# Optimization experiments

Hardware: AMD Instinct MI355X
Metric: run time of the kernel (lower is better)

The kernel has to match this reference:

```python
import jax, jax.numpy as jnp
import numpy as np

B, S, IN_DIM, OUT_DIM = 4, 2048, 1024, 1024
NEG = -9e15

def _xavier(key, shape, gain=1.414):
    fan_in, fan_out = shape[0], shape[1]
    a = gain * np.sqrt(6.0 / (fan_in + fan_out))
    return jax.random.uniform(key, shape, jnp.float32, -a, a)

def setup_inputs() -> dict:
    key = jax.random.key(0)
    ks = jax.random.split(key, 8)
    x = jax.random.normal(ks[0], (B, S, IN_DIM), jnp.float32)
    W_query = _xavier(ks[1], (IN_DIM, OUT_DIM))
    W_key = _xavier(ks[2], (IN_DIM, OUT_DIM))
    W_value = _xavier(ks[3], (IN_DIM, OUT_DIM))
    # torch Linear default init (kaiming-uniform-ish); values don't matter for correctness baseline
    W1 = _xavier(ks[4], (OUT_DIM + IN_DIM, OUT_DIM), gain=1.0)
    b1 = jnp.zeros((OUT_DIM,), jnp.float32)
    W2 = _xavier(ks[5], (OUT_DIM, OUT_DIM), gain=1.0)
    b2 = jnp.zeros((OUT_DIM,), jnp.float32)
    return {"x": x, "W_query": W_query, "W_key": W_key, "W_value": W_value,
            "W1": W1, "b1": b1, "W2": W2, "b2": b2}

def reference(x, W_query, W_key, W_value, W1, b1, W2, b2):
    # QKV projections: [B,S,in] @ [in,out] -> [B,S,out]
    q = jnp.einsum('bsi,io->bso', x, W_query)
    k = jnp.einsum('bsi,io->bso', x, W_key)
    v = jnp.einsum('bsi,io->bso', x, W_value)
    scale = 1.0 / jnp.sqrt(jnp.float32(OUT_DIM))
    e = jnp.einsum('bqd,bkd->bqk', q, k) * scale  # [B,S,S]
    causal = jnp.tril(jnp.ones((S, S), jnp.float32))  # mask > 0 keeps lower triangle
    attn = jnp.where(causal > 0, e, jnp.float32(NEG))
    attn = jax.nn.softmax(attn, axis=2)
    # dropout: eval mode (train=False) -> identity
    out = jnp.einsum('bqk,bkd->bqd', attn, v)  # [B,S,out]
    h = jnp.concatenate([out, x], axis=-1)  # [B,S,out+in]
    h = jax.nn.relu(jnp.einsum('bsf,fo->bso', h, W1) + b1)
    return jnp.einsum('bsf,fo->bso', h, W2) + b2
```

## Files before the change

### kernel.cpp

```cpp
#include <hip/hip_runtime.h>
#include <stdint.h>

typedef __attribute__((ext_vector_type(8))) short short8;
typedef __attribute__((ext_vector_type(4))) short short4v;
typedef __attribute__((ext_vector_type(4))) float f32x4;

__device__ __forceinline__ unsigned short f32_to_bf16(float f) {
    unsigned int u = __float_as_uint(f);
    u += 0x7FFFu + ((u >> 16) & 1u);
    return (unsigned short)(u >> 16);
}

__device__ __forceinline__ short8 load8_f32_as_bf16(const float* __restrict__ ap) {
    f32x4 f0 = *(const f32x4*)ap;
    f32x4 f1 = *(const f32x4*)(ap + 4);
    union { short8 s; unsigned short u[8]; } cv;
#pragma unroll
    for (int t = 0; t < 4; ++t) {
        cv.u[t]     = f32_to_bf16(f0[t]);
        cv.u[t + 4] = f32_to_bf16(f1[t]);
    }
    return cv.s;
}

__device__ __forceinline__ void gld_lds16(const void* g, void* l) {
    __builtin_amdgcn_global_load_lds(
        (const __attribute__((address_space(1))) unsigned int*)(unsigned long long)(uintptr_t)g,
        (__attribute__((address_space(3))) unsigned int*)(unsigned int)(uintptr_t)l,
        16, 0, 0);
}

template<int AMODE, int EPI, int SWIZ, bool KLIMIT, int MT>
__global__ __launch_bounds__(256, 4)
void gemm128(const unsigned short* __restrict__ A, const unsigned short* __restrict__ A2,
             int lda, int lda2, int ksplit,
             const unsigned short* __restrict__ B, int ldb,
             void* __restrict__ C, int ldc, int K,
             long aStride, long bStride, long cStride,
             const float* __restrict__ bias, long biasStride, float scale,
             void* __restrict__ C2, int ldc2)
{
    int z = blockIdx.z;
    int mblk, nblk;
    if (SWIZ == 6) {
        int x = blockIdx.x, yy = blockIdx.y;
        if (z < 2) { mblk = x * 8 + (yy & 7); nblk = yy >> 3; }
        else       { nblk = x * 8 + (yy & 7); mblk = yy >> 3; }
    } else {
        mblk = blockIdx.y;
        nblk = blockIdx.x;
    }
    int m0 = mblk * MT;
    int n0 = nblk * 128;

    const unsigned short* Ab;
    const unsigned short* Bb;
    if (SWIZ == 6) {
        if (z < 2) { Ab = A; Bb = B + (size_t)z * bStride; }
        else       { Ab = B + (size_t)2 * bStride; Bb = A; }
    } else {
        Ab = A + (size_t)z * aStride;
        Bb = B + (size_t)z * bStride;
    }

    __shared__ __align__(16) short As[MT * 64];
    __shared__ __align__(16) short Bs[128 * 64];

    int tid  = threadIdx.x;
    int lane = tid & 63, wid = tid >> 6;
    constexpr int MI = MT / 32;
    int wm = (wid & 1) * (MT / 2), wn = (wid >> 1) * 64;
    int fr = lane & 15, fq = lane >> 4;
    int sw0 = ((fq    ) ^ (fr & 7)) * 16;
    int sw1 = ((fq ^ 4) ^ (fr & 7)) * 16;

    int rS = tid >> 3;
    int cS = ((tid & 7) ^ (rS & 7)) * 8;
    char* AsB = (char*)As; char* BsB = (char*)Bs;

    int kend = KLIMIT ? min(K, m0 + MT) : K;

    f32x4 acc[MI][4];
#pragma unroll
    for (int i = 0; i < MI; ++i)
#pragma unroll
    for (int j = 0; j < 4; ++j) acc[i][j] = f32x4{0.f, 0.f, 0.f, 0.f};

    for (int k0 = 0; k0 < kend; k0 += 64) {
        const unsigned short* Asrc = Ab;
        int koff = k0, ldax = lda;
        if (AMODE == 2 && k0 >= ksplit) { Asrc = A2; koff = k0 - ksplit; ldax = lda2; }
        const unsigned short* pa = Asrc + (size_t)(m0 + rS) * ldax + koff + cS;
        const unsigned short* pb = Bb   + (size_t)(n0 + rS) * ldb  + k0   + cS;
#pragma unroll
        for (int t = 0; t < MT / 32; ++t)
            gld_lds16(pa + (size_t)(32 * t) * ldax, AsB + t * 4096 + tid * 16);
#pragma unroll
        for (int t = 0; t < 4; ++t)
            gld_lds16(pb + (size_t)(32 * t) * ldb,  BsB + t * 4096 + tid * 16);
        __syncthreads();

#pragma unroll
        for (int kh = 0; kh < 2; ++kh) {
            int sw = kh ? sw1 : sw0;
            short8 a[MI], b[4];
#pragma unroll
            for (int i = 0; i < MI; ++i)
                a[i] = *(const short8*)(AsB + (wm + i * 16 + fr) * 128 + sw);
#pragma unroll
            for (int j = 0; j < 4; ++j)
                b[j] = *(const short8*)(BsB + (wn + j * 16 + fr) * 128 + sw);
#pragma unroll
            for (int i = 0; i < MI; ++i)
#pragma unroll
            for (int j = 0; j < 4; ++j)
                acc[i][j] = __builtin_amdgcn_mfma_f32_16x16x32_bf16(a[i], b[j], acc[i][j], 0, 0, 0);
        }
        __syncthreads();
    }

    if (EPI == 0) {
        unsigned short* Cz; int ldcz;
        if (SWIZ == 6 && z >= 2) { Cz = (unsigned short*)C2; ldcz = ldc2; }
        else { Cz = (unsigned short*)C + (size_t)z * cStride; ldcz = ldc; }
#pragma unroll
        for (int i = 0; i < MI; ++i)
#pragma unroll
        for (int j = 0; j < 4; ++j)
#pragma unroll
        for (int r = 0; r < 4; ++r) {
            int row = m0 + wm + i * 16 + fq * 4 + r;
            int col = n0 + wn + j * 16 + fr;
            Cz[(size_t)row * ldcz + col] = f32_to_bf16(acc[i][j][r]);
        }
    }
}

template<int AMODE, int EPI, int SWIZ, bool KLIMIT>
__global__ __launch_bounds__(256, 2)
void gemmdb(const unsigned short* __restrict__ A, const unsigned short* __restrict__ A2,
            int lda, int lda2, int ksplit,
            const unsigned short* __restrict__ B, int ldb,
            void* __restrict__ C, int ldc, int K,
            long aStride, long bStride, long cStride,
            const float* __restrict__ bias, long biasStride, float scale)
{
    int z = blockIdx.z;
    int mblk, nblk;
    if (SWIZ == 1) {
        int lin = blockIdx.y * gridDim.x + blockIdx.x;
        int mchunk = gridDim.y >> 3;
        int xcd = lin & 7, idx = lin >> 3;
        mblk = xcd * mchunk + idx % mchunk;
        nblk = idx / mchunk;
    } else if (SWIZ == 5) {
        int x = blockIdx.x;
        int per = (int)gridDim.x >> 3;
        x = (x & 7) * per + (x >> 3);
        int a = (int)sqrtf(2.f * (float)x + 1.f);
        if (a > 15) a = 15;
        while (a < 15 && ((a + 1) * (a + 2) / 2) <= x) ++a;
        while (a > 0 && (a * (a + 1) / 2) > x) --a;
        mblk = a;
        nblk = x - a * (a + 1) / 2;
    } else if (SWIZ == 7) {
        int glin = (int)blockIdx.z * 128 + (int)blockIdx.y * 8 + (int)blockIdx.x;
        int xcd = glin & 7;
        int s   = glin >> 3;
        z = xcd >> 1;
        int h  = xcd & 1;
        int jm = s & 7;
        nblk   = s >> 3;
        mblk   = (jm & 1) ? (15 - h - (jm >> 1) * 2) : ((jm >> 1) * 2 + h);
    } else {
        mblk = blockIdx.y;
        nblk = blockIdx.x;
    }
    int m0 = mblk * 128;
    int n0 = nblk * 128;

    const unsigned short* Ab = A + (size_t)z * aStride;
    const unsigned short* Bb = B + (size_t)z * bStride;

    __shared__ __align__(16) char lds[65536];

    int tid  = threadIdx.x;
    int lane = tid & 63, wid = tid >> 6;
    int wm = (wid & 1) * 64, wn = (wid >> 1) * 64;
    int fr = lane & 15, fq = lane >> 4;
    int sw0 = ((fq    ) ^ (fr & 7)) * 16;
    int sw1 = ((fq ^ 4) ^ (fr & 7)) * 16;

    int rS = tid >> 3;
    int cS = ((tid & 7) ^ (rS & 7)) * 8;

    int kend = KLIMIT ? min(K, m0 + 128) : K;
    int NT = kend >> 6;

    f32x4 acc[4][4];
#pragma unroll
    for (int i = 0; i < 4; ++i)
#pragma unroll
    for (int j = 0; j < 4; ++j) acc[i][j] = f32x4{0.f, 0.f, 0.f, 0.f};

    auto STAGE = [&](int kt) {
        char* dst = lds + (kt & 1) * 32768;
        const unsigned short* Asrc = Ab; int koff = kt << 6; int ldax = lda;
        if (AMODE == 2 && koff >= ksplit) { Asrc = A2; koff -= ksplit; ldax = lda2; }
        const unsigned short* pa = Asrc + (size_t)(m0 + rS) * ldax + koff + cS;
        const unsigned short* pb = Bb   + (size_t)(n0 + rS) * ldb + (kt << 6) + cS;
#pragma unroll
        for (int u = 0; u < 4; ++u)
            gld_lds16(pa + (size_t)(32 * u) * ldax, dst + u * 4096 + tid * 16);
#pragma unroll
        for (int u = 0; u < 4; ++u)
            gld_lds16(pb + (size_t)(32 * u) * ldb, dst + 16384 + u * 4096 + tid * 16);
    };

    STAGE(0);
    for (int t = 0; t < NT; ++t) {
        if (t + 1 < NT) {
            STAGE(t + 1);
            asm volatile("s_waitcnt vmcnt(8)" ::: "memory");
        } else {
            asm volatile("s_waitcnt vmcnt(0)" ::: "memory");
        }
        __builtin_amdgcn_s_barrier();
        __builtin_amdgcn_sched_barrier(0);
        const char* AsB = (const char*)lds + (t & 1) * 32768;
        const char* BsB = AsB + 16384;
#pragma unroll
        for (int kh = 0; kh < 2; ++kh) {
            int sw = kh ? sw1 : sw0;
            short8 a[4], b[4];
#pragma unroll
            for (int i = 0; i < 4; ++i)
                a[i] = *(const short8*)(AsB + (wm + i * 16 + fr) * 128 + sw);
#pragma unroll
            for (int j = 0; j < 4; ++j)
                b[j] = *(const short8*)(BsB + (wn + j * 16 + fr) * 128 + sw);
            __builtin_amdgcn_s_setprio(1);
#pragma unroll
            for (int i = 0; i < 4; ++i)
#pragma unroll
            for (int j = 0; j < 4; ++j)
                acc[i][j] = __builtin_amdgcn_mfma_f32_16x16x32_bf16(a[i], b[j], acc[i][j], 0, 0, 0);
            __builtin_amdgcn_s_setprio(0);
        }
        __builtin_amdgcn_s_barrier();
        __builtin_amdgcn_sched_barrier(0);
        asm volatile("" ::: "memory");
    }

    if (EPI == 6) {
        unsigned short* Cz = (unsigned short*)C + (size_t)z * cStride;
        float* rs = const_cast<float*>(bias) + z * biasStride;
#pragma unroll
        for (int i = 0; i < 4; ++i)
#pragma unroll
        for (int r = 0; r < 4; ++r) {
            int row = m0 + wm + i * 16 + fq * 4 + r;
            float s = 0.f;
#pragma unroll
            for (int j = 0; j < 4; ++j) {
                int col = n0 + wn + j * 16 + fr;
                float e = (col <= row) ? __expf(acc[i][j][r] * scale - 16.f) : 0.f;
                s += e;
                Cz[(size_t)row * ldc + col] = f32_to_bf16(e);
            }
            s += __shfl_xor(s, 1);
            s += __shfl_xor(s, 2);
            s += __shfl_xor(s, 4);
            s += __shfl_xor(s, 8);
            if (fr == 0) atomicAdd(&rs[row], s);
        }
    } else if (EPI == 4) {
        unsigned short* Cz = (unsigned short*)C + (size_t)z * cStride;
#pragma unroll
        for (int i = 0; i < 4; ++i)
#pragma unroll
        for (int r = 0; r < 4; ++r) {
            int row = m0 + wm + i * 16 + fq * 4 + r;
            float inv = 1.f / bias[z * biasStride + row];
#pragma unroll
            for (int j = 0; j < 4; ++j) {
                int col = n0 + wn + j * 16 + fr;
                Cz[(size_t)row * ldc + col] = f32_to_bf16(acc[i][j][r] * inv);
            }
        }
    } else {
#pragma unroll
        for (int i = 0; i < 4; ++i)
#pragma unroll
        for (int j = 0; j < 4; ++j)
#pragma unroll
        for (int r = 0; r < 4; ++r) {
            int row = m0 + wm + i * 16 + fq * 4 + r;
            int col = n0 + wn + j * 16 + fr;
            float v = acc[i][j][r];
            if (EPI == 2) {
                v += bias[col];
                v = v > 0.f ? v : 0.f;
                ((unsigned short*)C + (size_t)z * cStride)[(size_t)row * ldc + col] = f32_to_bf16(v);
            } else {
                ((float*)C + (size_t)z * cStride)[(size_t)row * ldc + col] = v + bias[col];
            }
        }
    }
}

__device__ __forceinline__ void transpose_tile64(const float* __restrict__ in,
                                                 unsigned short* __restrict__ out,
                                                 int rows, int cols, int bx, int by, int tid)
{
    __shared__ float t[64][65];
    int tx = tid & 15, ty = tid >> 4;
    int r0 = by * 64, c0 = bx * 64;
#pragma unroll
    for (int i = 0; i < 4; ++i) {
        f32x4 v = *(const f32x4*)(in + (size_t)(r0 + ty + i * 16) * cols + c0 + tx * 4);
#pragma unroll
        for (int j = 0; j < 4; ++j) t[ty + i * 16][tx * 4 + j] = v[j];
    }
    __syncthreads();
#pragma unroll
    for (int i = 0; i < 4; ++i) {
        union { short4v s; unsigned short u[4]; } o;
#pragma unroll
        for (int j = 0; j < 4; ++j) o.u[j] = f32_to_bf16(t[tx * 4 + j][ty + i * 16]);
        *(short4v*)(out + (size_t)(c0 + ty + i * 16) * rows + r0 + tx * 4) = o.s;
    }
}

__global__ __launch_bounds__(256)
void prep_kernel(const float* __restrict__ x,
                 const float* __restrict__ Wq, const float* __restrict__ Wk,
                 const float* __restrict__ Wv, const float* __restrict__ W1,
                 const float* __restrict__ W2,
                 unsigned short* __restrict__ xb, unsigned short* __restrict__ WT,
                 unsigned short* __restrict__ W1T, unsigned short* __restrict__ W2T,
                 float* __restrict__ rsum)
{
    int idx = blockIdx.x;
    int tid = threadIdx.x;
    if (idx < 1024) {
#pragma unroll
        for (int it = 0; it < 4; ++it) {
            size_t i = ((size_t)idx * 4 + it) * 2048 + (size_t)tid * 8;
            *(short8*)(xb + i) = load8_f32_as_bf16(x + i);
        }
    } else if (idx < 1792) {
        int t = idx - 1024;
        int w = t >> 8; t &= 255;
        const float* in = w == 0 ? Wq : (w == 1 ? Wk : Wv);
        transpose_tile64(in, WT + (size_t)w * 1024 * 1024, 1024, 1024,
                         t & 15, t >> 4, tid);
    } else if (idx < 2304) {
        int t = idx - 1792;
        transpose_tile64(W1, W1T, 2048, 1024, t & 15, t >> 4, tid);
    } else if (idx < 2560) {
        int t = idx - 2304;
        transpose_tile64(W2, W2T, 1024, 1024, t & 15, t >> 4, tid);
    } else {
        int t = idx - 2560;
        f32x4 zero = {0.f, 0.f, 0.f, 0.f};
        float* p = rsum + ((size_t)t * 256 + tid) * 8;
        *(f32x4*)p = zero;
        *(f32x4*)(p + 4) = zero;
    }
}

extern "C" void kernel_launch(void* const* d_in, const int* in_sizes, int n_in,
                              void* d_out, int out_size, void* d_ws, size_t ws_size,
                              hipStream_t stream)
{
    const float* x  = (const float*)d_in[0];
    const float* Wq = (const float*)d_in[1];
    const float* Wk = (const float*)d_in[2];
    const float* Wv = (const float*)d_in[3];
    const float* W1 = (const float*)d_in[4];
    const float* b1 = (const float*)d_in[5];
    const float* W2 = (const float*)d_in[6];
    const float* b2 = (const float*)d_in[7];
    float* out = (float*)d_out;

    size_t off = 0;
    auto alloc = [&](size_t bytes) {
        char* r = (char*)d_ws + off;
        off += (bytes + 255) & ~(size_t)255;
        return r;
    };
    const size_t TOK = (size_t)8192 * 1024;
    unsigned short* WT   = (unsigned short*)alloc((size_t)3072 * 1024 * 2);
    unsigned short* W1T  = (unsigned short*)alloc((size_t)1024 * 2048 * 2);
    unsigned short* W2T  = (unsigned short*)alloc((size_t)1024 * 1024 * 2);
    unsigned short* xb   = (unsigned short*)alloc(TOK * 2);
    unsigned short* vT   = (unsigned short*)alloc((size_t)1024 * 8192 * 2);
    unsigned short* attn = (unsigned short*)alloc(TOK * 2);
    float*          rsum = (float*)         alloc((size_t)4 * 2048 * 4);
    unsigned short* q    = (unsigned short*)alloc(TOK * 2);
    unsigned short* k    = (unsigned short*)alloc(TOK * 2);
    unsigned short* S    = (unsigned short*)alloc((size_t)4 * 2048 * 2048 * 2);
    unsigned short* h1   = S;

    prep_kernel<<<2564, 256, 0, stream>>>(x, Wq, Wk, Wv, W1, W2, xb, WT, W1T, W2T, rsum);

    gemm128<0, 0, 6, false, 128><<<dim3(8, 64, 3), 256, 0, stream>>>(
        xb, nullptr, 1024, 0, 0, WT, 1024, q, 1024, 1024,
        0, (long)1024 * 1024, (long)TOK, nullptr, 0, 0.f, vT, 8192);

    gemmdb<0, 6, 5, false><<<dim3(136, 1, 4), 256, 0, stream>>>(
        q, nullptr, 1024, 0, 0, k, 1024, S, 2048, 1024,
        (long)2048 * 1024, (long)2048 * 1024, (long)2048 * 2048, rsum, 2048, 0.03125f);

    gemmdb<0, 4, 7, true><<<dim3(8, 16, 4), 256, 0, stream>>>(
        S, nullptr, 2048, 0, 0, vT, 8192, attn, 1024, 2048,
        (long)2048 * 2048, (long)2048, (long)2048 * 1024, rsum, 2048, 0.f);

    gemmdb<2, 2, 1, false><<<dim3(8, 64, 1), 256, 0, stream>>>(
        attn, xb, 1024, 1024, 1024, W1T, 2048, h1, 1024, 2048,
        0, 0, 0, b1, 0, 0.f);

    gemmdb<0, 3, 1, false><<<dim3(8, 64, 1), 256, 0, stream>>>(
        h1, nullptr, 1024, 0, 0, W2T, 1024, out, 1024, 1024,
        0, 0, 0, b2, 0, 0.f);
}
```

Baseline: 287.5 us.

## Use 256x128 tiles with 8 waves and triple-buffered LDS pipeline

Replaces the 128x128 double-buffered GEMM with a 512-thread kernel that computes 256x128 tiles and keeps a three-stage LDS ring, so loads are issued two k-steps ahead and only one barrier is needed per iteration. It also remaps the causal-triangle and attention-times-V block schedules onto the larger tiles, and removes unused template paths from the QKV GEMM. The larger tiles raise data reuse per block and deepen prefetch. In exchange they need 144KB of LDS per block and halve the number of blocks, which can lower occupancy and waste more work on partially masked causal tiles.

```diff
diff --git a/kernel.cpp b/kernel.cpp
--- a/kernel.cpp
+++ b/kernel.cpp
@@ -30,38 +30,29 @@
         16, 0, 0);
 }
 
-template<int AMODE, int EPI, int SWIZ, bool KLIMIT, int MT>
+template<int EPI, int SWIZ, int MT>
 __global__ __launch_bounds__(256, 4)
-void gemm128(const unsigned short* __restrict__ A, const unsigned short* __restrict__ A2,
-             int lda, int lda2, int ksplit,
+void gemm128(const unsigned short* __restrict__ A,
+             int lda,
              const unsigned short* __restrict__ B, int ldb,
              void* __restrict__ C, int ldc, int K,
-             long aStride, long bStride, long cStride,
-             const float* __restrict__ bias, long biasStride, float scale,
+             long bStride, long cStride,
              void* __restrict__ C2, int ldc2)
 {
     int z = blockIdx.z;
     int mblk, nblk;
-    if (SWIZ == 6) {
+    {
         int x = blockIdx.x, yy = blockIdx.y;
         if (z < 2) { mblk = x * 8 + (yy & 7); nblk = yy >> 3; }
         else       { nblk = x * 8 + (yy & 7); mblk = yy >> 3; }
-    } else {
-        mblk = blockIdx.y;
-        nblk = blockIdx.x;
     }
     int m0 = mblk * MT;
     int n0 = nblk * 128;
 
     const unsigned short* Ab;
     const unsigned short* Bb;
-    if (SWIZ == 6) {
-        if (z < 2) { Ab = A; Bb = B + (size_t)z * bStride; }
-        else       { Ab = B + (size_t)2 * bStride; Bb = A; }
-    } else {
-        Ab = A + (size_t)z * aStride;
-        Bb = B + (size_t)z * bStride;
-    }
+    if (z < 2) { Ab = A; Bb = B + (size_t)z * bStride; }
+    else       { Ab = B + (size_t)2 * bStride; Bb = A; }
 
     __shared__ __align__(16) short As[MT * 64];
     __shared__ __align__(16) short Bs[128 * 64];
@@ -78,23 +69,18 @@
     int cS = ((tid & 7) ^ (rS & 7)) * 8;
     char* AsB = (char*)As; char* BsB = (char*)Bs;
 
-    int kend = KLIMIT ? min(K, m0 + MT) : K;
-
     f32x4 acc[MI][4];
 #pragma unroll
     for (int i = 0; i < MI; ++i)
 #pragma unroll
     for (int j = 0; j < 4; ++j) acc[i][j] = f32x4{0.f, 0.f, 0.f, 0.f};
 
-    for (int k0 = 0; k0 < kend; k0 += 64) {
-        const unsigned short* Asrc = Ab;
-        int koff = k0, ldax = lda;
-        if (AMODE == 2 && k0 >= ksplit) { Asrc = A2; koff = k0 - ksplit; ldax = lda2; }
-        const unsigned short* pa = Asrc + (size_t)(m0 + rS) * ldax + koff + cS;
-        const unsigned short* pb = Bb   + (size_t)(n0 + rS) * ldb  + k0   + cS;
+    for (int k0 = 0; k0 < K; k0 += 64) {
+        const unsigned short* pa = Ab + (size_t)(m0 + rS) * lda + k0 + cS;
+        const unsigned short* pb = Bb + (size_t)(n0 + rS) * ldb + k0 + cS;
 #pragma unroll
         for (int t = 0; t < MT / 32; ++t)
-            gld_lds16(pa + (size_t)(32 * t) * ldax, AsB + t * 4096 + tid * 16);
+            gld_lds16(pa + (size_t)(32 * t) * lda, AsB + t * 4096 + tid * 16);
 #pragma unroll
         for (int t = 0; t < 4; ++t)
             gld_lds16(pb + (size_t)(32 * t) * ldb,  BsB + t * 4096 + tid * 16);
@@ -119,26 +105,24 @@
         __syncthreads();
     }
 
-    if (EPI == 0) {
-        unsigned short* Cz; int ldcz;
-        if (SWIZ == 6 && z >= 2) { Cz = (unsigned short*)C2; ldcz = ldc2; }
-        else { Cz = (unsigned short*)C + (size_t)z * cStride; ldcz = ldc; }
-#pragma unroll
-        for (int i = 0; i < MI; ++i)
-#pragma unroll
-        for (int j = 0; j < 4; ++j)
-#pragma unroll
-        for (int r = 0; r < 4; ++r) {
-            int row = m0 + wm + i * 16 + fq * 4 + r;
-            int col = n0 + wn + j * 16 + fr;
-            Cz[(size_t)row * ldcz + col] = f32_to_bf16(acc[i][j][r]);
-        }
+    unsigned short* Cz; int ldcz;
+    if (z >= 2) { Cz = (unsigned short*)C2; ldcz = ldc2; }
+    else { Cz = (unsigned short*)C + (size_t)z * cStride; ldcz = ldc; }
+#pragma unroll
+    for (int i = 0; i < MI; ++i)
+#pragma unroll
+    for (int j = 0; j < 4; ++j)
+#pragma unroll
+    for (int r = 0; r < 4; ++r) {
+        int row = m0 + wm + i * 16 + fq * 4 + r;
+        int col = n0 + wn + j * 16 + fr;
+        Cz[(size_t)row * ldcz + col] = f32_to_bf16(acc[i][j][r]);
     }
 }
 
 template<int AMODE, int EPI, int SWIZ, bool KLIMIT>
-__global__ __launch_bounds__(256, 2)
-void gemmdb(const unsigned short* __restrict__ A, const unsigned short* __restrict__ A2,
+__global__ __launch_bounds__(512, 2)
+void gemm8p(const unsigned short* __restrict__ A, const unsigned short* __restrict__ A2,
             int lda, int lda2, int ksplit,
             const unsigned short* __restrict__ B, int ldb,
             void* __restrict__ C, int ldc, int K,
@@ -149,44 +133,38 @@
     int mblk, nblk;
     if (SWIZ == 1) {
         int lin = blockIdx.y * gridDim.x + blockIdx.x;
-        int mchunk = gridDim.y >> 3;
         int xcd = lin & 7, idx = lin >> 3;
-        mblk = xcd * mchunk + idx % mchunk;
-        nblk = idx / mchunk;
+        int mch = (int)gridDim.y >> 3;
+        mblk = xcd * mch + idx % mch;
+        nblk = idx / mch;
     } else if (SWIZ == 5) {
         int x = blockIdx.x;
-        int per = (int)gridDim.x >> 3;
-        x = (x & 7) * per + (x >> 3);
-        int a = (int)sqrtf(2.f * (float)x + 1.f);
-        if (a > 15) a = 15;
-        while (a < 15 && ((a + 1) * (a + 2) / 2) <= x) ++a;
-        while (a > 0 && (a * (a + 1) / 2) > x) --a;
-        mblk = a;
-        nblk = x - a * (a + 1) / 2;
-    } else if (SWIZ == 7) {
-        int glin = (int)blockIdx.z * 128 + (int)blockIdx.y * 8 + (int)blockIdx.x;
-        int xcd = glin & 7;
-        int s   = glin >> 3;
-        z = xcd >> 1;
-        int h  = xcd & 1;
-        int jm = s & 7;
-        nblk   = s >> 3;
-        mblk   = (jm & 1) ? (15 - h - (jm >> 1) * 2) : ((jm >> 1) * 2 + h);
+        int i = 0;
+        while (i < 7 && (i + 1) * (i + 2) <= x) ++i;
+        mblk = i;
+        nblk = x - i * (i + 1);
+    } else if (SWIZ == 8) {
+        int p = blockIdx.x;
+        int s = (int)blockIdx.z * 8 + (int)blockIdx.y;
+        nblk = s >> 2;
+        int msel = (s >> 1) & 1, zsel = s & 1;
+        z    = 2 * (p & 1) + zsel;
+        mblk = msel ? 7 - (p >> 1) : (p >> 1);
     } else {
         mblk = blockIdx.y;
         nblk = blockIdx.x;
     }
-    int m0 = mblk * 128;
-    int n0 = nblk * 128;
+    int m0 = mblk * 256, n0 = nblk * 128;
 
     const unsigned short* Ab = A + (size_t)z * aStride;
     const unsigned short* Bb = B + (size_t)z * bStride;
 
-    __shared__ __align__(16) char lds[65536];
+    constexpr int TILE = 49152;
+    __shared__ __align__(16) char lds[3 * TILE];
 
     int tid  = threadIdx.x;
     int lane = tid & 63, wid = tid >> 6;
-    int wm = (wid & 1) * 64, wn = (wid >> 1) * 64;
+    int wm = (wid & 3) * 64, wn = (wid >> 2) * 64;
     int fr = lane & 15, fq = lane >> 4;
     int sw0 = ((fq    ) ^ (fr & 7)) * 16;
     int sw1 = ((fq ^ 4) ^ (fr & 7)) * 16;
@@ -194,7 +172,7 @@
     int rS = tid >> 3;
     int cS = ((tid & 7) ^ (rS & 7)) * 8;
 
-    int kend = KLIMIT ? min(K, m0 + 128) : K;
+    int kend = KLIMIT ? min(K, m0 + 256) : K;
     int NT = kend >> 6;
 
     f32x4 acc[4][4];
@@ -203,32 +181,33 @@
 #pragma unroll
     for (int j = 0; j < 4; ++j) acc[i][j] = f32x4{0.f, 0.f, 0.f, 0.f};
 
-    auto STAGE = [&](int kt) {
-        char* dst = lds + (kt & 1) * 32768;
-        const unsigned short* Asrc = Ab; int koff = kt << 6; int ldax = lda;
-        if (AMODE == 2 && koff >= ksplit) { Asrc = A2; koff -= ksplit; ldax = lda2; }
+    auto STAGE = [&](int t, int slot) {
+        int k0 = t << 6;
+        char* dst = lds + slot * TILE;
+        const unsigned short* Asrc = Ab; int koff = k0, ldax = lda;
+        if (AMODE == 2 && k0 >= ksplit) { Asrc = A2; koff = k0 - ksplit; ldax = lda2; }
         const unsigned short* pa = Asrc + (size_t)(m0 + rS) * ldax + koff + cS;
-        const unsigned short* pb = Bb   + (size_t)(n0 + rS) * ldb + (kt << 6) + cS;
+        const unsigned short* pb = Bb   + (size_t)(n0 + rS) * ldb  + k0   + cS;
 #pragma unroll
         for (int u = 0; u < 4; ++u)
-            gld_lds16(pa + (size_t)(32 * u) * ldax, dst + u * 4096 + tid * 16);
-#pragma unroll
-        for (int u = 0; u < 4; ++u)
-            gld_lds16(pb + (size_t)(32 * u) * ldb, dst + 16384 + u * 4096 + tid * 16);
+            gld_lds16(pa + (size_t)(64 * u) * ldax, dst + u * 8192 + tid * 16);
+#pragma unroll
+        for (int u = 0; u < 2; ++u)
+            gld_lds16(pb + (size_t)(64 * u) * ldb, dst + 32768 + u * 8192 + tid * 16);
     };
 
-    STAGE(0);
+    STAGE(0, 0);
+    STAGE(1, 1);
+    asm volatile("s_waitcnt vmcnt(6)" ::: "memory");
+    __builtin_amdgcn_s_barrier();
+    __builtin_amdgcn_sched_barrier(0);
+    asm volatile("" ::: "memory");
+
+    int sc = 0, ss = 2;
     for (int t = 0; t < NT; ++t) {
-        if (t + 1 < NT) {
-            STAGE(t + 1);
-            asm volatile("s_waitcnt vmcnt(8)" ::: "memory");
-        } else {
-            asm volatile("s_waitcnt vmcnt(0)" ::: "memory");
-        }
-        __builtin_amdgcn_s_barrier();
-        __builtin_amdgcn_sched_barrier(0);
-        const char* AsB = (const char*)lds + (t & 1) * 32768;
-        const char* BsB = AsB + 16384;
+        if (t + 2 < NT) STAGE(t + 2, ss);
+        const char* AsB = (const char*)(lds + sc * TILE);
+        const char* BsB = AsB + 32768;
 #pragma unroll
         for (int kh = 0; kh < 2; ++kh) {
             int sw = kh ? sw1 : sw0;
@@ -247,9 +226,15 @@
                 acc[i][j] = __builtin_amdgcn_mfma_f32_16x16x32_bf16(a[i], b[j], acc[i][j], 0, 0, 0);
             __builtin_amdgcn_s_setprio(0);
         }
-        __builtin_amdgcn_s_barrier();
-        __builtin_amdgcn_sched_barrier(0);
-        asm volatile("" ::: "memory");
+        if (t + 1 < NT) {
+            if (t + 2 < NT) { asm volatile("s_waitcnt vmcnt(6)" ::: "memory"); }
+            else            { asm volatile("s_waitcnt vmcnt(0)" ::: "memory"); }
+            __builtin_amdgcn_s_barrier();
+            __builtin_amdgcn_sched_barrier(0);
+            asm volatile("" ::: "memory");
+        }
+        sc = sc == 2 ? 0 : sc + 1;
+        ss = ss == 2 ? 0 : ss + 1;
     }
 
     if (EPI == 6) {
@@ -301,9 +286,9 @@
             if (EPI == 2) {
                 v += bias[col];
                 v = v > 0.f ? v : 0.f;
-                ((unsigned short*)C + (size_t)z * cStride)[(size_t)row * ldc + col] = f32_to_bf16(v);
+                ((unsigned short*)C)[(size_t)row * ldc + col] = f32_to_bf16(v);
             } else {
-                ((float*)C + (size_t)z * cStride)[(size_t)row * ldc + col] = v + bias[col];
+                ((float*)C)[(size_t)row * ldc + col] = v + bias[col];
             }
         }
     }
@@ -405,23 +390,25 @@
 
     prep_kernel<<<2564, 256, 0, stream>>>(x, Wq, Wk, Wv, W1, W2, xb, WT, W1T, W2T, rsum);
 
-    gemm128<0, 0, 6, false, 128><<<dim3(8, 64, 3), 256, 0, stream>>>(
-        xb, nullptr, 1024, 0, 0, WT, 1024, q, 1024, 1024,
-        0, (long)1024 * 1024, (long)TOK, nullptr, 0, 0.f, vT, 8192);
-
-    gemmdb<0, 6, 5, false><<<dim3(136, 1, 4), 256, 0, stream>>>(
+    gemm128<0, 6, 128><<<dim3(8, 64, 3), 256, 0, stream>>>(
+        xb, 1024, WT, 1024, q, 1024, 1024,
+        (long)1024 * 1024, (long)TOK, vT, 8192);
+
+    gemm8p<0, 6, 5, false><<<dim3(72, 1, 4), 512, 0, stream>>>(
         q, nullptr, 1024, 0, 0, k, 1024, S, 2048, 1024,
-        (long)2048 * 1024, (long)2048 * 1024, (long)2048 * 2048, rsum, 2048, 0.03125f);
-
-    gemmdb<0, 4, 7, true><<<dim3(8, 16, 4), 256, 0, stream>>>(
+        (long)2048 * 1024, (long)2048 * 1024, (long)2048 * 2048,
+        rsum, 2048, 0.03125f);
+
+    gemm8p<0, 4, 8, true><<<dim3(8, 8, 4), 512, 0, stream>>>(
         S, nullptr, 2048, 0, 0, vT, 8192, attn, 1024, 2048,
-        (long)2048 * 2048, (long)2048, (long)2048 * 1024, rsum, 2048, 0.f);
-
-    gemmdb<2, 2, 1, false><<<dim3(8, 64, 1), 256, 0, stream>>>(
+        (long)2048 * 2048, (long)2048, (long)2048 * 1024,
+        rsum, 2048, 0.f);
+
+    gemm8p<2, 2, 1, false><<<dim3(8, 32, 1), 512, 0, stream>>>(
         attn, xb, 1024, 1024, 1024, W1T, 2048, h1, 1024, 2048,
         0, 0, 0, b1, 0, 0.f);
 
-    gemmdb<0, 3, 1, false><<<dim3(8, 64, 1), 256, 0, stream>>>(
+    gemm8p<0, 3, 1, false><<<dim3(8, 32, 1), 512, 0, stream>>>(
         h1, nullptr, 1024, 0, 0, W2T, 1024, out, 1024, 1024,
         0, 0, 0, b2, 0, 0.f);
 }
```

Result: slower. 293.9 us (+2.2%).
